# Performance work log

Measured on AMD Instinct MI355X. Metric: run time of the kernel, lower is better.

## Reference

```python
import jax, jax.numpy as jnp
import numpy as np

MARGIN = 0.3


def setup_inputs() -> dict:
    key = jax.random.key(0)
    k1, k2 = jax.random.split(key)
    B, D, NCLS = 4096, 2048, 64
    inputs = jax.random.normal(k1, (B, D), dtype=jnp.float32)
    targets = jax.random.randint(k2, (B,), 0, NCLS, dtype=jnp.int64)
    return {"inputs": inputs, "targets": targets}


def _triplet_loss(inputs, targets, margin):
    sq = jnp.sum(inputs * inputs, axis=1)  # [B]
    distmat = sq[:, None] + sq[None, :] - 2.0 * (inputs @ inputs.T)  # [B, B]
    distmat = jnp.sqrt(jnp.clip(distmat, 1e-12, None))
    same = targets[None, :] == targets[:, None]  # [B, B]; includes diagonal
    neg_inf = jnp.float32(-jnp.inf)
    pos_inf = jnp.float32(jnp.inf)
    d_pos = jnp.max(jnp.where(same, distmat, neg_inf), axis=1)  # hardest positive
    d_neg = jnp.min(jnp.where(same, pos_inf, distmat), axis=1)  # hardest negative
    # MarginRankingLoss(x1=d_neg, x2=d_pos, y=1): mean(relu(-(d_neg - d_pos) + margin))
    return jnp.mean(jax.nn.relu(d_pos - d_neg + margin))


def reference(inputs, targets):
    return _triplet_loss(inputs, targets, MARGIN)
```

## Files before the change

kernel.cpp:

```cpp
#include <hip/hip_runtime.h>
#include <hip/hip_bf16.h>


typedef __attribute__((ext_vector_type(8))) short short8;
typedef __attribute__((ext_vector_type(4))) float f32x4;
using bf16 = __hip_bfloat16;

#define BN_ROWS 4096
#define D_DIM   2048
#define TILE    128
#define BK      64
#define NSTEP   (D_DIM / BK)
#define NB      (BN_ROWS / TILE)
#define NBLK    (NB * (NB + 1) / 2)
#define MARGIN  0.3f

__device__ __forceinline__ void gload16(const bf16* g, bf16* l) {
  __builtin_amdgcn_global_load_lds(
      (const __attribute__((address_space(1))) void*)g,
      (__attribute__((address_space(3))) void*)l, 16, 0, 0);
}

__global__ __launch_bounds__(256) void prep_kernel(
    const float* __restrict__ x, bf16* __restrict__ xb, float* __restrict__ sqv,
    unsigned* __restrict__ pos, unsigned* __restrict__ neg) {
  const int row = blockIdx.x;
  const int t = threadIdx.x;
  const float4* xr = (const float4*)(x + (size_t)row * D_DIM);
  bf16* xbr = xb + (size_t)row * D_DIM;
  float s = 0.f;
  #pragma unroll
  for (int p = 0; p < 2; ++p) {
    const int idx = t + p * 256;
    float4 a = xr[idx];
    s += a.x * a.x + a.y * a.y + a.z * a.z + a.w * a.w;
    union { ushort4 v; bf16 h[4]; } u;
    u.h[0] = __float2bfloat16(a.x);
    u.h[1] = __float2bfloat16(a.y);
    u.h[2] = __float2bfloat16(a.z);
    u.h[3] = __float2bfloat16(a.w);
    *(ushort4*)(xbr + (size_t)idx * 4) = u.v;
  }
  #pragma unroll
  for (int o = 32; o; o >>= 1) s += __shfl_down(s, o, 64);
  __shared__ float red[4];
  if ((t & 63) == 0) red[t >> 6] = s;
  __syncthreads();
  if (t == 0) {
    sqv[row] = red[0] + red[1] + red[2] + red[3];
    pos[row] = 0u;
    neg[row] = 0x7F800000u;
  }
}

__global__ __launch_bounds__(512) void gram_kernel(
    const bf16* __restrict__ xb, const float* __restrict__ sqv,
    const int* __restrict__ tgt, unsigned* __restrict__ pos,
    unsigned* __restrict__ neg) {
  __shared__ bf16 As[2][TILE * BK];
  __shared__ bf16 Bs[2][TILE * BK];
  const int t = threadIdx.x;
  const int wave = t >> 6, lane = t & 63;

  const int id = (blockIdx.x & 7) * (NBLK / 8) + (blockIdx.x >> 3);

  int by = (int)(0.5f * (65.0f - sqrtf(4225.0f - 8.0f * (float)id)));
  while (by * NB - (by * (by - 1)) / 2 > id) --by;
  while ((by + 1) * NB - ((by + 1) * by) / 2 <= id) ++by;
  const int bx = by + (id - (by * NB - (by * (by - 1)) / 2));
  const int rowBase = by * TILE;
  const int colBase = bx * TILE;

  const int wr = wave >> 2, wc = wave & 3;
  const int lhi = lane >> 4, llo = lane & 15;

  f32x4 acc[4][2];
  #pragma unroll
  for (int m = 0; m < 4; ++m)
    #pragma unroll
    for (int n = 0; n < 2; ++n) acc[m][n] = (f32x4){0.f, 0.f, 0.f, 0.f};

  const int srow = lane >> 3;
  const int swz = (lane & 7) ^ srow;

  auto stage = [&](int buf, int step) {
    const size_t kcol = (size_t)step * BK + (size_t)swz * 8;
    #pragma unroll
    for (int c = 0; c < 2; ++c) {
      const int chunk = wave * 2 + c;
      gload16(xb + (size_t)(rowBase + chunk * 8 + srow) * D_DIM + kcol,
              &As[buf][chunk * 512]);
      gload16(xb + (size_t)(colBase + chunk * 8 + srow) * D_DIM + kcol,
              &Bs[buf][chunk * 512]);
    }
  };

  auto compute = [&](int buf) {
    #pragma unroll
    for (int kk = 0; kk < 2; ++kk) {
      short8 af[4], bfr[2];
      #pragma unroll
      for (int m = 0; m < 4; ++m) {
        const int row = wr * 64 + m * 16 + llo;
        const int c16 = (kk * 4 + lhi) ^ (row & 7);
        af[m] = *(const short8*)(&As[buf][row * 64 + c16 * 8]);
      }
      #pragma unroll
      for (int n = 0; n < 2; ++n) {
        const int row = wc * 32 + n * 16 + llo;
        const int c16 = (kk * 4 + lhi) ^ (row & 7);
        bfr[n] = *(const short8*)(&Bs[buf][row * 64 + c16 * 8]);
      }
      #pragma unroll
      for (int m = 0; m < 4; ++m)
        #pragma unroll
        for (int n = 0; n < 2; ++n)
          acc[m][n] = __builtin_amdgcn_mfma_f32_16x16x32_bf16(
              af[m], bfr[n], acc[m][n], 0, 0, 0);
    }
  };

  stage(0, 0);
  for (int s = 0; s < NSTEP - 1; ++s) {
    stage((s + 1) & 1, s + 1);
    asm volatile("s_waitcnt vmcnt(4)\n\ts_barrier" ::: "memory");
    compute(s & 1);
    asm volatile("s_barrier" ::: "memory");
  }
  asm volatile("s_waitcnt vmcnt(0)\n\ts_barrier" ::: "memory");
  compute((NSTEP - 1) & 1);

  const float inf = __uint_as_float(0x7F800000u);
  float sqj[2];
  int tgj[2];
  #pragma unroll
  for (int n = 0; n < 2; ++n) {
    const int j = colBase + wc * 32 + n * 16 + llo;
    sqj[n] = sqv[j];
    tgj[n] = tgt[j];
  }
  float colP[2] = {0.f, 0.f};
  float colN[2] = {inf, inf};

  #pragma unroll
  for (int m = 0; m < 4; ++m) {
    #pragma unroll
    for (int r = 0; r < 4; ++r) {
      const int i = rowBase + wr * 64 + m * 16 + lhi * 4 + r;
      const float sqi = sqv[i];
      const int tgi = tgt[i];
      float pm = 0.0f, nm = inf;
      #pragma unroll
      for (int n = 0; n < 2; ++n) {
        const float g = acc[m][n][r];
        const float d2 = sqi + sqj[n] - 2.0f * g;
        const float d = sqrtf(fmaxf(d2, 1e-12f));
        if (tgj[n] == tgi) {
          pm = fmaxf(pm, d);
          colP[n] = fmaxf(colP[n], d);
        } else {
          nm = fminf(nm, d);
          colN[n] = fminf(colN[n], d);
        }
      }
      #pragma unroll
      for (int o = 1; o < 16; o <<= 1) {
        pm = fmaxf(pm, __shfl_xor(pm, o, 64));
        nm = fminf(nm, __shfl_xor(nm, o, 64));
      }
      if (llo == 0) {
        atomicMax(pos + i, __float_as_uint(pm));
        atomicMin(neg + i, __float_as_uint(nm));
      }
    }
  }
  #pragma unroll
  for (int n = 0; n < 2; ++n) {
    float cp = colP[n], cn = colN[n];
    cp = fmaxf(cp, __shfl_xor(cp, 16, 64));
    cp = fmaxf(cp, __shfl_xor(cp, 32, 64));
    cn = fminf(cn, __shfl_xor(cn, 16, 64));
    cn = fminf(cn, __shfl_xor(cn, 32, 64));
    if (lane < 16) {
      const int j = colBase + wc * 32 + n * 16 + llo;
      atomicMax(pos + j, __float_as_uint(cp));
      atomicMin(neg + j, __float_as_uint(cn));
    }
  }
}

__global__ __launch_bounds__(1024) void loss_kernel(
    const unsigned* __restrict__ pos, const unsigned* __restrict__ neg,
    float* __restrict__ out) {
  const int t = threadIdx.x;
  float s = 0.f;
  for (int i = t; i < BN_ROWS; i += 1024) {
    const float dp = __uint_as_float(pos[i]);
    const float dn = __uint_as_float(neg[i]);
    const float v = dp - dn + MARGIN;
    s += v > 0.f ? v : 0.f;
  }
  #pragma unroll
  for (int o = 32; o; o >>= 1) s += __shfl_down(s, o, 64);
  __shared__ float red[16];
  if ((t & 63) == 0) red[t >> 6] = s;
  __syncthreads();
  if (t < 16) {
    float v = red[t];
    #pragma unroll
    for (int o = 8; o; o >>= 1) v += __shfl_down(v, o, 16);
    if (t == 0) out[0] = v * (1.0f / (float)BN_ROWS);
  }
}

extern "C" void kernel_launch(void* const* d_in, const int* in_sizes, int n_in,
                              void* d_out, int out_size, void* d_ws, size_t ws_size,
                              hipStream_t stream) {
  const float* x = (const float*)d_in[0];
  const int* tgt = (const int*)d_in[1];
  float* out = (float*)d_out;

  char* ws = (char*)d_ws;
  bf16* xb = (bf16*)ws;
  float* sqv = (float*)(ws + (size_t)BN_ROWS * D_DIM * 2);
  unsigned* pos = (unsigned*)((char*)sqv + BN_ROWS * 4);
  unsigned* neg = (unsigned*)((char*)pos + BN_ROWS * 4);

  prep_kernel<<<BN_ROWS, 256, 0, stream>>>(x, xb, sqv, pos, neg);
  gram_kernel<<<NBLK, 512, 0, stream>>>(xb, sqv, tgt, pos, neg);
  loss_kernel<<<1, 1024, 0, stream>>>(pos, neg, out);
}
```

Measured before the change: 161.1 us.

## Load A operand directly from global into registers, keep only B in LDS

The Gram kernel stops staging the row (A) tile through shared memory. Each wave now reads its A fragments straight from global memory into registers, prefetched one K-step ahead, while the column (B) tile stays double-buffered in LDS via async global-to-LDS loads. The launch bounds also request more resident blocks per CU. This halves LDS usage and removes the A-side LDS reads, but the four column-waves that share a row block each fetch the same A data, which multiplies global/L2 traffic. The tighter occupancy request can also cause register pressure or spills.

```diff
diff --git a/kernel.cpp b/kernel.cpp
--- a/kernel.cpp
+++ b/kernel.cpp
@@ -53,11 +53,10 @@
   }
 }
 
-__global__ __launch_bounds__(512) void gram_kernel(
+__global__ __launch_bounds__(512, 4) void gram_kernel(
     const bf16* __restrict__ xb, const float* __restrict__ sqv,
     const int* __restrict__ tgt, unsigned* __restrict__ pos,
     unsigned* __restrict__ neg) {
-  __shared__ bf16 As[2][TILE * BK];
   __shared__ bf16 Bs[2][TILE * BK];
   const int t = threadIdx.x;
   const int wave = t >> 6, lane = t & 63;
@@ -83,52 +82,56 @@
   const int srow = lane >> 3;
   const int swz = (lane & 7) ^ srow;
 
-  auto stage = [&](int buf, int step) {
+  auto stageB = [&](int buf, int step) {
     const size_t kcol = (size_t)step * BK + (size_t)swz * 8;
     #pragma unroll
     for (int c = 0; c < 2; ++c) {
       const int chunk = wave * 2 + c;
-      gload16(xb + (size_t)(rowBase + chunk * 8 + srow) * D_DIM + kcol,
-              &As[buf][chunk * 512]);
       gload16(xb + (size_t)(colBase + chunk * 8 + srow) * D_DIM + kcol,
               &Bs[buf][chunk * 512]);
     }
   };
 
-  auto compute = [&](int buf) {
-    #pragma unroll
-    for (int kk = 0; kk < 2; ++kk) {
-      short8 af[4], bfr[2];
+  auto loadA_kk = [&](int step, int kk, short8* af) {
+    const size_t kc = (size_t)step * BK + (size_t)(kk * 32 + lhi * 8);
+    #pragma unroll
+    for (int m = 0; m < 4; ++m) {
+      const int row = rowBase + wr * 64 + m * 16 + llo;
+      af[m] = *(const short8*)(xb + (size_t)row * D_DIM + kc);
+    }
+  };
+
+  auto compute_kk = [&](int buf, int kk, const short8* af) {
+    short8 bfr[2];
+    #pragma unroll
+    for (int n = 0; n < 2; ++n) {
+      const int row = wc * 32 + n * 16 + llo;
+      const int c16 = (kk * 4 + lhi) ^ (row & 7);
+      bfr[n] = *(const short8*)(&Bs[buf][row * 64 + c16 * 8]);
+    }
+    #pragma unroll
+    for (int m = 0; m < 4; ++m)
       #pragma unroll
-      for (int m = 0; m < 4; ++m) {
-        const int row = wr * 64 + m * 16 + llo;
-        const int c16 = (kk * 4 + lhi) ^ (row & 7);
-        af[m] = *(const short8*)(&As[buf][row * 64 + c16 * 8]);
-      }
-      #pragma unroll
-      for (int n = 0; n < 2; ++n) {
-        const int row = wc * 32 + n * 16 + llo;
-        const int c16 = (kk * 4 + lhi) ^ (row & 7);
-        bfr[n] = *(const short8*)(&Bs[buf][row * 64 + c16 * 8]);
-      }
-      #pragma unroll
-      for (int m = 0; m < 4; ++m)
-        #pragma unroll
-        for (int n = 0; n < 2; ++n)
-          acc[m][n] = __builtin_amdgcn_mfma_f32_16x16x32_bf16(
-              af[m], bfr[n], acc[m][n], 0, 0, 0);
-    }
+      for (int n = 0; n < 2; ++n)
+        acc[m][n] = __builtin_amdgcn_mfma_f32_16x16x32_bf16(
+            af[m], bfr[n], acc[m][n], 0, 0, 0);
   };
 
-  stage(0, 0);
+  short8 af0[4], af1[4];
+  stageB(0, 0);
+  loadA_kk(0, 0, af0);
+  loadA_kk(0, 1, af1);
+  asm volatile("s_waitcnt vmcnt(0)\n\ts_barrier" ::: "memory");
   for (int s = 0; s < NSTEP - 1; ++s) {
-    stage((s + 1) & 1, s + 1);
-    asm volatile("s_waitcnt vmcnt(4)\n\ts_barrier" ::: "memory");
-    compute(s & 1);
-    asm volatile("s_barrier" ::: "memory");
-  }
-  asm volatile("s_waitcnt vmcnt(0)\n\ts_barrier" ::: "memory");
-  compute((NSTEP - 1) & 1);
+    stageB((s + 1) & 1, s + 1);
+    compute_kk(s & 1, 0, af0);
+    loadA_kk(s + 1, 0, af0);
+    compute_kk(s & 1, 1, af1);
+    loadA_kk(s + 1, 1, af1);
+    asm volatile("s_waitcnt vmcnt(8)\n\ts_barrier" ::: "memory");
+  }
+  compute_kk((NSTEP - 1) & 1, 0, af0);
+  compute_kk((NSTEP - 1) & 1, 1, af1);
 
   const float inf = __uint_as_float(0x7F800000u);
   float sqj[2];
```

Measured after the change: 282.9 us. +75.7%, slower.
